# Optimization experiments

Measured on AMD Instinct MI355X. Metric: run time of the kernel, lower is better.

## Reference

```python
import jax, jax.numpy as jnp
import numpy as np

K = 4  # top-k nearest neighbors


def setup_inputs() -> dict:
    key = jax.random.key(0)
    k1, k2, k3 = jax.random.split(key, 3)
    N, D, M = 784, 512, 65536  # N_patches (28*28), feature dim, memory bank size
    query = jax.random.normal(k1, (N, D), dtype=jnp.float32)
    memory_bank = jax.random.normal(k2, (M, D), dtype=jnp.float32)
    # fcn: Conv2d(in=2*D=1024, out=1, kernel=3, padding=1)
    fan_in = 2 * D * 9
    fcn_w = jax.random.normal(k3, (1, 2 * D, 3, 3), dtype=jnp.float32) / np.sqrt(fan_in)
    fcn_b = jnp.zeros((1,), dtype=jnp.float32)
    return {"query": query, "memory_bank": memory_bank, "fcn_w": fcn_w, "fcn_b": fcn_b}


def reference(query, memory_bank, fcn_w, fcn_b):
    # pairwise L2 distances (torch.cdist p=2): [N, M]
    q2 = jnp.sum(query * query, axis=1, keepdims=True)           # [N, 1]
    m2 = jnp.sum(memory_bank * memory_bank, axis=1)              # [M]
    d2 = q2 + m2[None, :] - 2.0 * (query @ memory_bank.T)        # [N, M]
    dist = jnp.sqrt(jnp.maximum(d2, 0.0))
    # top-k smallest distances -> indices
    _, topk_idx = jax.lax.top_k(-dist, K)                        # [N, K]
    neighbors = memory_bank[topk_idx]                            # [N, K, D] gather
    neighbor_mean = jnp.mean(neighbors, axis=1)                  # [N, D]
    combined = jnp.concatenate([query, neighbor_mean], axis=1)   # [N, 2D]
    n, dim = combined.shape
    s = int(np.sqrt(n))                                          # 28
    x = combined.T.reshape(1, dim, s, s)                         # [1, 2D, 28, 28]
    out = jax.lax.conv_general_dilated(
        x, fcn_w, window_strides=(1, 1), padding=((1, 1), (1, 1)),
        dimension_numbers=("NCHW", "OIHW", "NCHW"))
    return out + fcn_b[None, :, None, None]                      # [1, 1, 28, 28]
```

## Files before the change

kernel.cpp:

```cpp
#include <hip/hip_runtime.h>
#include <hip/hip_bf16.h>
#include <stdint.h>

#define DIMS 512
#define NQ 784
#define QPAD 832
#define NM 65536
#define NTILE 13
#define NGROUP 2048
#define RESCORE 16
#define COLSTRIDE 1040

typedef float f32x4 __attribute__((ext_vector_type(4)));
typedef short bf16x8 __attribute__((ext_vector_type(8)));

__device__ __forceinline__ unsigned short f2bf(float x) {
    unsigned u = __float_as_uint(x);
    u += 0x7fffu + ((u >> 16) & 1u);
    return (unsigned short)(u >> 16);
}
__device__ __forceinline__ unsigned umn(unsigned a, unsigned b) { return a < b ? a : b; }
__device__ __forceinline__ unsigned umx(unsigned a, unsigned b) { return a > b ? a : b; }

__global__ __launch_bounds__(256) void prep_query(const float* __restrict__ q,
                                                  unsigned short* __restrict__ qbuf) {
    int i = (blockIdx.x * 256 + threadIdx.x) * 4;
    int row = i >> 9;
    ushort4 o = make_ushort4(0, 0, 0, 0);
    if (row < NQ) {
        float4 v = *(const float4*)(q + i);
        o.x = f2bf(v.x); o.y = f2bf(v.y); o.z = f2bf(v.z); o.w = f2bf(v.w);
    }
    *(ushort4*)(qbuf + i) = o;
}

__global__ __launch_bounds__(512, 1) void score_kernel(
    const float* __restrict__ bank,
    const unsigned short* __restrict__ qbuf,
    uint2* __restrict__ cand)
{
    __shared__ __align__(16) char bt[2][64 * COLSTRIDE];
    __shared__ float m2s[256];

    const int wg = blockIdx.x;
    const int t = threadIdx.x;
    const int v = t >> 6;
    const int lane = t & 63;
    const int lo = lane & 15;
    const int kg = lane >> 4;

#define STAGE(buf, tile)                                                                  \
    do {                                                                                  \
        _Pragma("unroll")                                                                 \
        for (int j = 0; j < 8; ++j) {                                                     \
            const int col = v * 8 + j;                                                    \
            const unsigned short* src =                                                   \
                qbuf + ((size_t)((tile) * 64 + col)) * DIMS + lane * 8;                   \
            __builtin_amdgcn_global_load_lds(                                             \
                (const __attribute__((address_space(1))) unsigned*)src,                   \
                (__attribute__((address_space(3))) unsigned*)(&bt[buf][col * COLSTRIDE]), \
                16, 0, 0);                                                                \
        }                                                                                 \
    } while (0)

    STAGE(0, 0);

    bf16x8 areg[2][16];
    float m2p[2];
    #pragma unroll
    for (int m = 0; m < 2; ++m) {
        const float* rp = bank + ((size_t)(wg * 256 + v * 32 + m * 16 + lo)) * DIMS + kg * 8;
        float ss = 0.f;
        #pragma unroll
        for (int ks = 0; ks < 16; ++ks) {
            float4 x = *(const float4*)(rp + ks * 32);
            float4 y = *(const float4*)(rp + ks * 32 + 4);
            ss += x.x * x.x + x.y * x.y + x.z * x.z + x.w * x.w;
            ss += y.x * y.x + y.y * y.y + y.z * y.z + y.w * y.w;
            union { bf16x8 v8; unsigned u[4]; } fr;
            __hip_bfloat162 h0 = __float22bfloat162_rn(make_float2(x.x, x.y));
            __hip_bfloat162 h1 = __float22bfloat162_rn(make_float2(x.z, x.w));
            __hip_bfloat162 h2 = __float22bfloat162_rn(make_float2(y.x, y.y));
            __hip_bfloat162 h3 = __float22bfloat162_rn(make_float2(y.z, y.w));
            fr.u[0] = *reinterpret_cast<unsigned*>(&h0);
            fr.u[1] = *reinterpret_cast<unsigned*>(&h1);
            fr.u[2] = *reinterpret_cast<unsigned*>(&h2);
            fr.u[3] = *reinterpret_cast<unsigned*>(&h3);
            areg[m][ks] = fr.v8;
        }
        m2p[m] = ss;
    }
    #pragma unroll
    for (int m = 0; m < 2; ++m) {
        m2p[m] += __shfl_xor(m2p[m], 16);
        m2p[m] += __shfl_xor(m2p[m], 32);
    }
    if (lane < 16) {
        m2s[v * 32 + lane] = m2p[0];
        m2s[v * 32 + 16 + lane] = m2p[1];
    }
    __syncthreads();
    f32x4 seed0, seed1;
    #pragma unroll
    for (int j = 0; j < 4; ++j) {
        seed0[j] = -0.5f * (1024.0f + m2s[v * 32 + kg * 4 + j]);
        seed1[j] = -0.5f * (1024.0f + m2s[v * 32 + 16 + kg * 4 + j]);
    }

    asm volatile("s_waitcnt vmcnt(0)" ::: "memory");
    __syncthreads();

    #pragma unroll 1
    for (int tile = 0; tile < NTILE; ++tile) {
        const int cur = tile & 1;
        if (tile + 1 < NTILE) STAGE(cur ^ 1, tile + 1);

        const char* B = &bt[cur][0];
        const int ntpEnd = (tile == NTILE - 1) ? 1 : 2;
        #pragma unroll 1
        for (int ntp = 0; ntp < ntpEnd; ++ntp) {
            const char* pb0 = B + (ntp * 32 + lo) * COLSTRIDE + kg * 16;
            const char* pb1 = pb0 + 16 * COLSTRIDE;
            f32x4 a00 = seed0, a01 = seed1, a10 = seed0, a11 = seed1;
            #pragma unroll
            for (int ks = 0; ks < 16; ++ks) {
                bf16x8 b0 = *(const bf16x8*)(pb0 + ks * 64);
                bf16x8 b1 = *(const bf16x8*)(pb1 + ks * 64);
                a00 = __builtin_amdgcn_mfma_f32_16x16x32_bf16(areg[0][ks], b0, a00, 0, 0, 0);
                a01 = __builtin_amdgcn_mfma_f32_16x16x32_bf16(areg[1][ks], b0, a01, 0, 0, 0);
                a10 = __builtin_amdgcn_mfma_f32_16x16x32_bf16(areg[0][ks], b1, a10, 0, 0, 0);
                a11 = __builtin_amdgcn_mfma_f32_16x16x32_bf16(areg[1][ks], b1, a11, 0, 0, 0);
            }
            #pragma unroll
            for (int n = 0; n < 2; ++n) {
                unsigned v1 = 0xFFFFFFFFu, v2 = 0xFFFFFFFFu;
                const f32x4& am0 = n ? a10 : a00;
                const f32x4& am1 = n ? a11 : a01;
                #pragma unroll
                for (int j = 0; j < 4; ++j) {
                    float s0 = -2.0f * am0[j];
                    unsigned u0 = (__float_as_uint(s0) & ~31u) | (unsigned)(kg * 4 + j);
                    unsigned t0 = umx(v1, u0);
                    v1 = umn(v1, u0);
                    v2 = umn(v2, t0);
                    float s1 = -2.0f * am1[j];
                    unsigned u1 = (__float_as_uint(s1) & ~31u) | (unsigned)(16 + kg * 4 + j);
                    unsigned t1 = umx(v1, u1);
                    v1 = umn(v1, u1);
                    v2 = umn(v2, t1);
                }
                #pragma unroll
                for (int off = 16; off <= 32; off <<= 1) {
                    unsigned o1 = (unsigned)__shfl_xor((int)v1, off);
                    unsigned o2 = (unsigned)__shfl_xor((int)v2, off);
                    unsigned mx = umx(v1, o1);
                    v1 = umn(v1, o1);
                    v2 = umn(umn(v2, o2), mx);
                }
                int col = tile * 64 + ntp * 32 + n * 16 + (lane & 15);
                if (lane < 16 && col < NQ)
                    cand[(size_t)(wg * 8 + v) * QPAD + col] = make_uint2(v1, v2);
            }
        }
        asm volatile("s_waitcnt vmcnt(0)" ::: "memory");
        __syncthreads();
    }
#undef STAGE
}

__global__ __launch_bounds__(256) void merge_kernel(
    const float* __restrict__ query, const float* __restrict__ bank,
    const uint2* __restrict__ cand, float* __restrict__ nm)
{
    const int row = blockIdx.x * 4 + (threadIdx.x >> 6);
    const int lane = threadIdx.x & 63;

    unsigned s0 = 0xFFFFFFFFu, s1 = 0xFFFFFFFFu, s2 = 0xFFFFFFFFu;
    unsigned s3 = 0xFFFFFFFFu, s4 = 0xFFFFFFFFu, s5 = 0xFFFFFFFFu;

#define INSERT(uu)                                  \
    do {                                            \
        unsigned tt = (uu), nv;                     \
        nv = umn(s0, tt); tt = umx(s0, tt); s0 = nv;\
        nv = umn(s1, tt); tt = umx(s1, tt); s1 = nv;\
        nv = umn(s2, tt); tt = umx(s2, tt); s2 = nv;\
        nv = umn(s3, tt); tt = umx(s3, tt); s3 = nv;\
        nv = umn(s4, tt); tt = umx(s4, tt); s4 = nv;\
        s5 = umn(s5, tt);                           \
    } while (0)

    #pragma unroll 4
    for (int j = 0; j < 32; ++j) {
        uint2 e = cand[((size_t)(lane * 32 + j)) * QPAD + row];
        unsigned jb = (unsigned)(j << 5);
        unsigned u0 = (e.x & ~0x3E0u) | jb;
        unsigned u1 = (e.y & ~0x3E0u) | jb;
        INSERT(u0);
        INSERT(u1);
    }
#undef INSERT

    int cidx[RESCORE];
    #pragma unroll
    for (int it = 0; it < RESCORE; ++it) {
        unsigned gm = s0;
        #pragma unroll
        for (int off = 1; off < 64; off <<= 1)
            gm = umn(gm, (unsigned)__shfl_xor((int)gm, off));
        unsigned long long bal = __ballot(s0 == gm);
        int wl = __ffsll((long long)bal) - 1;
        if (lane == wl) { s0 = s1; s1 = s2; s2 = s3; s3 = s4; s4 = s5; s5 = 0xFFFFFFFFu; }
        int g = wl * 32 + (int)((gm >> 5) & 31u);
        cidx[it] = g * 32 + (int)(gm & 31u);
    }

    const float* qr = query + (size_t)row * DIMS + lane * 8;
    float4 qx = *(const float4*)qr;
    float4 qy = *(const float4*)(qr + 4);
    double d2[RESCORE];
    #pragma unroll
    for (int c = 0; c < RESCORE; ++c) {
        const float* mr = bank + (size_t)cidx[c] * DIMS + lane * 8;
        float4 mx = *(const float4*)mr;
        float4 my = *(const float4*)(mr + 4);
        double s = 0.0;
        double dd;
        dd = (double)qx.x - (double)mx.x; s += dd * dd;
        dd = (double)qx.y - (double)mx.y; s += dd * dd;
        dd = (double)qx.z - (double)mx.z; s += dd * dd;
        dd = (double)qx.w - (double)mx.w; s += dd * dd;
        dd = (double)qy.x - (double)my.x; s += dd * dd;
        dd = (double)qy.y - (double)my.y; s += dd * dd;
        dd = (double)qy.z - (double)my.z; s += dd * dd;
        dd = (double)qy.w - (double)my.w; s += dd * dd;
        #pragma unroll
        for (int off = 1; off < 64; off <<= 1) s += __shfl_xor(s, off);
        d2[c] = s;
    }

    int sel[4];
    unsigned used = 0;
    #pragma unroll
    for (int k = 0; k < 4; ++k) {
        double bv = 1e300; int bidx = 1 << 30; int bc = 0;
        #pragma unroll
        for (int c = 0; c < RESCORE; ++c) {
            bool live = !((used >> c) & 1u);
            if (live && (d2[c] < bv || (d2[c] == bv && cidx[c] < bidx))) {
                bv = d2[c]; bidx = cidx[c]; bc = c;
            }
        }
        used |= 1u << bc;
        sel[k] = bidx;
    }

    const float* r0 = bank + (size_t)sel[0] * DIMS + lane * 8;
    const float* r1 = bank + (size_t)sel[1] * DIMS + lane * 8;
    const float* r2 = bank + (size_t)sel[2] * DIMS + lane * 8;
    const float* r3 = bank + (size_t)sel[3] * DIMS + lane * 8;
    float* dst = nm + (size_t)row * DIMS + lane * 8;
    #pragma unroll
    for (int h = 0; h < 2; ++h) {
        float4 a = *(const float4*)(r0 + h * 4);
        float4 b = *(const float4*)(r1 + h * 4);
        float4 c = *(const float4*)(r2 + h * 4);
        float4 d = *(const float4*)(r3 + h * 4);
        float4 o;
        o.x = 0.25f * (a.x + b.x + c.x + d.x);
        o.y = 0.25f * (a.y + b.y + c.y + d.y);
        o.z = 0.25f * (a.z + b.z + c.z + d.z);
        o.w = 0.25f * (a.w + b.w + c.w + d.w);
        *(float4*)(dst + h * 4) = o;
    }
}

__global__ __launch_bounds__(256) void conv_kernel(
    const float* __restrict__ query, const float* __restrict__ nm,
    const float* __restrict__ fw, const float* __restrict__ fb,
    float* __restrict__ out)
{
    __shared__ float red[256];
    int pix = blockIdx.x, t = threadIdx.x;
    int i = pix / 28, j = pix % 28;
    float acc = 0.f;
    for (int c = t; c < 1024; c += 256) {
        const float* wrow = fw + c * 9;
        for (int di = 0; di < 3; ++di) {
            int h = i + di - 1;
            if (h < 0 || h >= 28) continue;
            for (int dj = 0; dj < 3; ++dj) {
                int w = j + dj - 1;
                if (w < 0 || w >= 28) continue;
                int n = h * 28 + w;
                float x = (c < 512) ? query[(size_t)n * 512 + c]
                                    : nm[(size_t)n * 512 + (c - 512)];
                acc += x * wrow[di * 3 + dj];
            }
        }
    }
    red[t] = acc;
    __syncthreads();
    for (int s = 128; s; s >>= 1) {
        if (t < s) red[t] += red[t + s];
        __syncthreads();
    }
    if (t == 0) out[pix] = red[0] + fb[0];
}

extern "C" void kernel_launch(void* const* d_in, const int* in_sizes, int n_in,
                              void* d_out, int out_size, void* d_ws, size_t ws_size,
                              hipStream_t stream)
{
    const float* query = (const float*)d_in[0];
    const float* bank  = (const float*)d_in[1];
    const float* fw    = (const float*)d_in[2];
    const float* fb    = (const float*)d_in[3];
    float* out = (float*)d_out;

    char* ws = (char*)d_ws;
    unsigned short* qbuf = (unsigned short*)ws;
    uint2* cand = (uint2*)(ws + 851968);
    float* nm   = (float*)(ws + 851968 + 13631488);

    prep_query<<<QPAD * DIMS / 1024, 256, 0, stream>>>(query, qbuf);
    score_kernel<<<256, 512, 0, stream>>>(bank, qbuf, cand);
    merge_kernel<<<NQ / 4, 256, 0, stream>>>(query, bank, cand, nm);
    conv_kernel<<<NQ, 256, 0, stream>>>(query, nm, fw, fb, out);
}
```

Baseline: 128.6 us.

## Switch coarse distance scoring to FP8 MFMA with swizzled LDS and wider rescoring

The coarse bank-vs-query scoring GEMM now uses fp8 e4m3 operands and 16x16x32 fp8 MFMA instead of bf16, halving query staging bytes. An XOR swizzle replaces the padded LDS stride. Work is split into 512 workgroups of 256 threads at two per CU, with a manually unrolled tile loop and s_setprio around the MFMA bursts. To offset the coarser fp8 scores, the merge keeps 8 candidates per lane and rescores 32 candidates exactly in double, one candidate per lane pair, with selection through shared memory. The risk is that fp8 error drops true neighbours out of the candidate set, and the merge step does more work.

```diff
diff --git a/kernel.cpp b/kernel.cpp
--- a/kernel.cpp
+++ b/kernel.cpp
@@ -1,46 +1,53 @@
 #include <hip/hip_runtime.h>
-#include <hip/hip_bf16.h>
+#include <hip/hip_fp8.h>
 #include <stdint.h>
 
 #define DIMS 512
 #define NQ 784
 #define QPAD 832
-#define NM 65536
 #define NTILE 13
-#define NGROUP 2048
-#define RESCORE 16
-#define COLSTRIDE 1040
+#define RESCORE 32
 
 typedef float f32x4 __attribute__((ext_vector_type(4)));
-typedef short bf16x8 __attribute__((ext_vector_type(8)));
-
-__device__ __forceinline__ unsigned short f2bf(float x) {
-    unsigned u = __float_as_uint(x);
-    u += 0x7fffu + ((u >> 16) & 1u);
-    return (unsigned short)(u >> 16);
-}
+
 __device__ __forceinline__ unsigned umn(unsigned a, unsigned b) { return a < b ? a : b; }
 __device__ __forceinline__ unsigned umx(unsigned a, unsigned b) { return a > b ? a : b; }
 
+__device__ __forceinline__ unsigned pk4(float a, float b, float c, float d) {
+#if __has_builtin(__builtin_amdgcn_cvt_pk_fp8_f32)
+    int v = 0;
+    v = __builtin_amdgcn_cvt_pk_fp8_f32(a, b, v, false);
+    v = __builtin_amdgcn_cvt_pk_fp8_f32(c, d, v, true);
+    return (unsigned)v;
+#else
+    __hip_fp8_e4m3 x(a), y(b), z(c), w(d);
+    return (unsigned)x.__x | ((unsigned)y.__x << 8) | ((unsigned)z.__x << 16) | ((unsigned)w.__x << 24);
+#endif
+}
+
 __global__ __launch_bounds__(256) void prep_query(const float* __restrict__ q,
-                                                  unsigned short* __restrict__ qbuf) {
-    int i = (blockIdx.x * 256 + threadIdx.x) * 4;
-    int row = i >> 9;
-    ushort4 o = make_ushort4(0, 0, 0, 0);
-    if (row < NQ) {
-        float4 v = *(const float4*)(q + i);
-        o.x = f2bf(v.x); o.y = f2bf(v.y); o.z = f2bf(v.z); o.w = f2bf(v.w);
-    }
-    *(ushort4*)(qbuf + i) = o;
-}
-
-__global__ __launch_bounds__(512, 1) void score_kernel(
+                                                  char* __restrict__ qb8) {
+    int gid = blockIdx.x * 256 + threadIdx.x;
+    int col = gid >> 6;
+    int k0 = (gid & 63) * 8;
+    float4 a = make_float4(0.f, 0.f, 0.f, 0.f), b = a;
+    if (col < NQ) {
+        a = *(const float4*)(q + (size_t)col * DIMS + k0);
+        b = *(const float4*)(q + (size_t)col * DIMS + k0 + 4);
+    }
+    uint2 o;
+    o.x = pk4(a.x, a.y, a.z, a.w);
+    o.y = pk4(b.x, b.y, b.z, b.w);
+    *(uint2*)(qb8 + col * 512 + (k0 ^ ((col & 7) << 3))) = o;
+}
+
+__global__ __launch_bounds__(256, 2) void score_kernel(
     const float* __restrict__ bank,
-    const unsigned short* __restrict__ qbuf,
+    const char* __restrict__ qb8,
     uint2* __restrict__ cand)
 {
-    __shared__ __align__(16) char bt[2][64 * COLSTRIDE];
-    __shared__ float m2s[256];
+    __shared__ __align__(16) char bt[2][64 * 512];
+    __shared__ float m2s[128];
 
     const int wg = blockIdx.x;
     const int t = threadIdx.x;
@@ -49,27 +56,26 @@
     const int lo = lane & 15;
     const int kg = lane >> 4;
 
-#define STAGE(buf, tile)                                                                  \
-    do {                                                                                  \
-        _Pragma("unroll")                                                                 \
-        for (int j = 0; j < 8; ++j) {                                                     \
-            const int col = v * 8 + j;                                                    \
-            const unsigned short* src =                                                   \
-                qbuf + ((size_t)((tile) * 64 + col)) * DIMS + lane * 8;                   \
-            __builtin_amdgcn_global_load_lds(                                             \
-                (const __attribute__((address_space(1))) unsigned*)src,                   \
-                (__attribute__((address_space(3))) unsigned*)(&bt[buf][col * COLSTRIDE]), \
-                16, 0, 0);                                                                \
-        }                                                                                 \
+#define STAGE(BUF, TILE)                                                              \
+    do {                                                                              \
+        _Pragma("unroll")                                                             \
+        for (int j = 0; j < 8; ++j) {                                                 \
+            const int col = v * 16 + j * 2;                                           \
+            const char* src = qb8 + ((size_t)((TILE) * 64 + col)) * 512 + lane * 16;  \
+            __builtin_amdgcn_global_load_lds(                                         \
+                (const __attribute__((address_space(1))) unsigned*)src,               \
+                (__attribute__((address_space(3))) unsigned*)(&bt[BUF][col * 512]),   \
+                16, 0, 0);                                                            \
+        }                                                                             \
     } while (0)
 
     STAGE(0, 0);
 
-    bf16x8 areg[2][16];
+    long areg[2][16];
     float m2p[2];
     #pragma unroll
     for (int m = 0; m < 2; ++m) {
-        const float* rp = bank + ((size_t)(wg * 256 + v * 32 + m * 16 + lo)) * DIMS + kg * 8;
+        const float* rp = bank + ((size_t)(wg * 128 + v * 32 + m * 16 + lo)) * DIMS + kg * 8;
         float ss = 0.f;
         #pragma unroll
         for (int ks = 0; ks < 16; ++ks) {
@@ -77,16 +83,9 @@
             float4 y = *(const float4*)(rp + ks * 32 + 4);
             ss += x.x * x.x + x.y * x.y + x.z * x.z + x.w * x.w;
             ss += y.x * y.x + y.y * y.y + y.z * y.z + y.w * y.w;
-            union { bf16x8 v8; unsigned u[4]; } fr;
-            __hip_bfloat162 h0 = __float22bfloat162_rn(make_float2(x.x, x.y));
-            __hip_bfloat162 h1 = __float22bfloat162_rn(make_float2(x.z, x.w));
-            __hip_bfloat162 h2 = __float22bfloat162_rn(make_float2(y.x, y.y));
-            __hip_bfloat162 h3 = __float22bfloat162_rn(make_float2(y.z, y.w));
-            fr.u[0] = *reinterpret_cast<unsigned*>(&h0);
-            fr.u[1] = *reinterpret_cast<unsigned*>(&h1);
-            fr.u[2] = *reinterpret_cast<unsigned*>(&h2);
-            fr.u[3] = *reinterpret_cast<unsigned*>(&h3);
-            areg[m][ks] = fr.v8;
+            unsigned l32 = pk4(x.x, x.y, x.z, x.w);
+            unsigned h32 = pk4(y.x, y.y, y.z, y.w);
+            areg[m][ks] = (long)(((unsigned long long)h32 << 32) | l32);
         }
         m2p[m] = ss;
     }
@@ -99,72 +98,90 @@
         m2s[v * 32 + lane] = m2p[0];
         m2s[v * 32 + 16 + lane] = m2p[1];
     }
-    __syncthreads();
-    f32x4 seed0, seed1;
-    #pragma unroll
-    for (int j = 0; j < 4; ++j) {
-        seed0[j] = -0.5f * (1024.0f + m2s[v * 32 + kg * 4 + j]);
-        seed1[j] = -0.5f * (1024.0f + m2s[v * 32 + 16 + kg * 4 + j]);
-    }
 
     asm volatile("s_waitcnt vmcnt(0)" ::: "memory");
     __syncthreads();
 
+    f32x4 seed0, seed1;
+    #pragma unroll
+    for (int j = 0; j < 4; ++j) {
+        seed0[j] = -(512.0f + 0.5f * m2s[v * 32 + kg * 4 + j]);
+        seed1[j] = -(512.0f + 0.5f * m2s[v * 32 + 16 + kg * 4 + j]);
+    }
+
+    const char* pA0 = &bt[0][0] + lo * 512 + ((kg * 8) ^ ((lo & 7) << 3));
+    const char* pA1 = (const char*)((uintptr_t)pA0 ^ 32);
+
+#define KSLOOP(ACC, BUF, NTP)                                                              \
+    do {                                                                                   \
+        __builtin_amdgcn_s_setprio(1);                                                     \
+        _Pragma("unroll")                                                                  \
+        for (int ks = 0; ks < 16; ++ks) {                                                  \
+            const char* bs = (ks & 1) ? pA1 : pA0;                                         \
+            const int off = (BUF) * 32768 + (NTP) * 16384 + (ks >> 1) * 64;                \
+            long b0 = *(const long*)(bs + off);                                            \
+            long b1 = *(const long*)(bs + off + 8192);                                     \
+            ACC[0][0] = __builtin_amdgcn_mfma_f32_16x16x32_fp8_fp8(areg[0][ks], b0, ACC[0][0], 0, 0, 0); \
+            ACC[1][0] = __builtin_amdgcn_mfma_f32_16x16x32_fp8_fp8(areg[1][ks], b0, ACC[1][0], 0, 0, 0); \
+            ACC[0][1] = __builtin_amdgcn_mfma_f32_16x16x32_fp8_fp8(areg[0][ks], b1, ACC[0][1], 0, 0, 0); \
+            ACC[1][1] = __builtin_amdgcn_mfma_f32_16x16x32_fp8_fp8(areg[1][ks], b1, ACC[1][1], 0, 0, 0); \
+        }                                                                                  \
+        __builtin_amdgcn_s_setprio(0);                                                     \
+    } while (0)
+
+#define SEL(ACC, TILE, NTP)                                                                \
+    do {                                                                                   \
+        _Pragma("unroll")                                                                  \
+        for (int n = 0; n < 2; ++n) {                                                      \
+            unsigned v1 = 0xFFFFFFFFu, v2 = 0xFFFFFFFFu;                                   \
+            _Pragma("unroll")                                                              \
+            for (int m = 0; m < 2; ++m)                                                    \
+                _Pragma("unroll")                                                          \
+                for (int j = 0; j < 4; ++j) {                                              \
+                    unsigned u = ((__float_as_uint(ACC[m][n][j]) ^ 0x80000000u) & ~31u)    \
+                                 | (unsigned)(m * 16 + kg * 4 + j);                        \
+                    unsigned mx = umx(v1, u);                                              \
+                    v1 = umn(v1, u);                                                       \
+                    v2 = umn(v2, mx);                                                      \
+                }                                                                          \
+            _Pragma("unroll")                                                              \
+            for (int off = 16; off <= 32; off <<= 1) {                                     \
+                unsigned o1 = (unsigned)__shfl_xor((int)v1, off);                          \
+                unsigned o2 = (unsigned)__shfl_xor((int)v2, off);                          \
+                unsigned mx = umx(v1, o1);                                                 \
+                v1 = umn(v1, o1);                                                          \
+                v2 = umn(umn(v2, o2), mx);                                                 \
+            }                                                                              \
+            int col = (TILE) * 64 + (NTP) * 32 + n * 16 + lo;                              \
+            if (lane < 16 && col < NQ)                                                     \
+                cand[(size_t)(wg * 4 + v) * QPAD + col] = make_uint2(v1, v2);              \
+        }                                                                                  \
+    } while (0)
+
+#define TILEBODY(TILE, BUF)                                                                \
+    do {                                                                                   \
+        if ((TILE) + 1 < NTILE) STAGE((BUF) ^ 1, (TILE) + 1);                              \
+        f32x4 accP[2][2], accQ[2][2];                                                      \
+        accP[0][0] = seed0; accP[0][1] = seed0; accP[1][0] = seed1; accP[1][1] = seed1;    \
+        KSLOOP(accP, BUF, 0);                                                              \
+        accQ[0][0] = seed0; accQ[0][1] = seed0; accQ[1][0] = seed1; accQ[1][1] = seed1;    \
+        KSLOOP(accQ, BUF, 1);                                                              \
+        SEL(accP, TILE, 0);                                                                \
+        SEL(accQ, TILE, 1);                                                                \
+        asm volatile("s_waitcnt vmcnt(0)" ::: "memory");                                   \
+        __syncthreads();                                                                   \
+    } while (0)
+
     #pragma unroll 1
-    for (int tile = 0; tile < NTILE; ++tile) {
-        const int cur = tile & 1;
-        if (tile + 1 < NTILE) STAGE(cur ^ 1, tile + 1);
-
-        const char* B = &bt[cur][0];
-        const int ntpEnd = (tile == NTILE - 1) ? 1 : 2;
-        #pragma unroll 1
-        for (int ntp = 0; ntp < ntpEnd; ++ntp) {
-            const char* pb0 = B + (ntp * 32 + lo) * COLSTRIDE + kg * 16;
-            const char* pb1 = pb0 + 16 * COLSTRIDE;
-            f32x4 a00 = seed0, a01 = seed1, a10 = seed0, a11 = seed1;
-            #pragma unroll
-            for (int ks = 0; ks < 16; ++ks) {
-                bf16x8 b0 = *(const bf16x8*)(pb0 + ks * 64);
-                bf16x8 b1 = *(const bf16x8*)(pb1 + ks * 64);
-                a00 = __builtin_amdgcn_mfma_f32_16x16x32_bf16(areg[0][ks], b0, a00, 0, 0, 0);
-                a01 = __builtin_amdgcn_mfma_f32_16x16x32_bf16(areg[1][ks], b0, a01, 0, 0, 0);
-                a10 = __builtin_amdgcn_mfma_f32_16x16x32_bf16(areg[0][ks], b1, a10, 0, 0, 0);
-                a11 = __builtin_amdgcn_mfma_f32_16x16x32_bf16(areg[1][ks], b1, a11, 0, 0, 0);
-            }
-            #pragma unroll
-            for (int n = 0; n < 2; ++n) {
-                unsigned v1 = 0xFFFFFFFFu, v2 = 0xFFFFFFFFu;
-                const f32x4& am0 = n ? a10 : a00;
-                const f32x4& am1 = n ? a11 : a01;
-                #pragma unroll
-                for (int j = 0; j < 4; ++j) {
-                    float s0 = -2.0f * am0[j];
-                    unsigned u0 = (__float_as_uint(s0) & ~31u) | (unsigned)(kg * 4 + j);
-                    unsigned t0 = umx(v1, u0);
-                    v1 = umn(v1, u0);
-                    v2 = umn(v2, t0);
-                    float s1 = -2.0f * am1[j];
-                    unsigned u1 = (__float_as_uint(s1) & ~31u) | (unsigned)(16 + kg * 4 + j);
-                    unsigned t1 = umx(v1, u1);
-                    v1 = umn(v1, u1);
-                    v2 = umn(v2, t1);
-                }
-                #pragma unroll
-                for (int off = 16; off <= 32; off <<= 1) {
-                    unsigned o1 = (unsigned)__shfl_xor((int)v1, off);
-                    unsigned o2 = (unsigned)__shfl_xor((int)v2, off);
-                    unsigned mx = umx(v1, o1);
-                    v1 = umn(v1, o1);
-                    v2 = umn(umn(v2, o2), mx);
-                }
-                int col = tile * 64 + ntp * 32 + n * 16 + (lane & 15);
-                if (lane < 16 && col < NQ)
-                    cand[(size_t)(wg * 8 + v) * QPAD + col] = make_uint2(v1, v2);
-            }
-        }
-        asm volatile("s_waitcnt vmcnt(0)" ::: "memory");
-        __syncthreads();
-    }
+    for (int tt = 0; tt < 6; ++tt) {
+        TILEBODY(2 * tt, 0);
+        TILEBODY(2 * tt + 1, 1);
+    }
+    TILEBODY(12, 0);
+
+#undef TILEBODY
+#undef SEL
+#undef KSLOOP
 #undef STAGE
 }
 
@@ -172,35 +189,39 @@
     const float* __restrict__ query, const float* __restrict__ bank,
     const uint2* __restrict__ cand, float* __restrict__ nm)
 {
-    const int row = blockIdx.x * 4 + (threadIdx.x >> 6);
-    const int lane = threadIdx.x & 63;
-
-    unsigned s0 = 0xFFFFFFFFu, s1 = 0xFFFFFFFFu, s2 = 0xFFFFFFFFu;
-    unsigned s3 = 0xFFFFFFFFu, s4 = 0xFFFFFFFFu, s5 = 0xFFFFFFFFu;
-
-#define INSERT(uu)                                  \
-    do {                                            \
-        unsigned tt = (uu), nv;                     \
-        nv = umn(s0, tt); tt = umx(s0, tt); s0 = nv;\
-        nv = umn(s1, tt); tt = umx(s1, tt); s1 = nv;\
-        nv = umn(s2, tt); tt = umx(s2, tt); s2 = nv;\
-        nv = umn(s3, tt); tt = umx(s3, tt); s3 = nv;\
-        nv = umn(s4, tt); tt = umx(s4, tt); s4 = nv;\
-        s5 = umn(s5, tt);                           \
+    __shared__ double d2s[4][32];
+    __shared__ int    cis[4][32];
+
+    const int wv = threadIdx.x >> 6, lane = threadIdx.x & 63;
+    const int row = blockIdx.x * 4 + wv;
+
+    unsigned s0 = ~0u, s1 = ~0u, s2 = ~0u, s3 = ~0u;
+    unsigned s4 = ~0u, s5 = ~0u, s6 = ~0u, s7 = ~0u;
+
+#define INS(U)                                        \
+    do {                                              \
+        unsigned tt = (U), nv;                        \
+        nv = umn(s0, tt); tt = umx(s0, tt); s0 = nv;  \
+        nv = umn(s1, tt); tt = umx(s1, tt); s1 = nv;  \
+        nv = umn(s2, tt); tt = umx(s2, tt); s2 = nv;  \
+        nv = umn(s3, tt); tt = umx(s3, tt); s3 = nv;  \
+        nv = umn(s4, tt); tt = umx(s4, tt); s4 = nv;  \
+        nv = umn(s5, tt); tt = umx(s5, tt); s5 = nv;  \
+        nv = umn(s6, tt); tt = umx(s6, tt); s6 = nv;  \
+        s7 = umn(s7, tt);                             \
     } while (0)
 
     #pragma unroll 4
     for (int j = 0; j < 32; ++j) {
         uint2 e = cand[((size_t)(lane * 32 + j)) * QPAD + row];
         unsigned jb = (unsigned)(j << 5);
-        unsigned u0 = (e.x & ~0x3E0u) | jb;
-        unsigned u1 = (e.y & ~0x3E0u) | jb;
-        INSERT(u0);
-        INSERT(u1);
-    }
-#undef INSERT
-
-    int cidx[RESCORE];
+        INS((e.x & ~0x3E0u) | jb);
+        INS((e.y & ~0x3E0u) | jb);
+    }
+#undef INS
+
+    const int myC = lane & 31;
+    int myCand = 0;
     #pragma unroll
     for (int it = 0; it < RESCORE; ++it) {
         unsigned gm = s0;
@@ -209,55 +230,48 @@
             gm = umn(gm, (unsigned)__shfl_xor((int)gm, off));
         unsigned long long bal = __ballot(s0 == gm);
         int wl = __ffsll((long long)bal) - 1;
-        if (lane == wl) { s0 = s1; s1 = s2; s2 = s3; s3 = s4; s4 = s5; s5 = 0xFFFFFFFFu; }
-        int g = wl * 32 + (int)((gm >> 5) & 31u);
-        cidx[it] = g * 32 + (int)(gm & 31u);
-    }
-
-    const float* qr = query + (size_t)row * DIMS + lane * 8;
-    float4 qx = *(const float4*)qr;
-    float4 qy = *(const float4*)(qr + 4);
-    double d2[RESCORE];
-    #pragma unroll
-    for (int c = 0; c < RESCORE; ++c) {
-        const float* mr = bank + (size_t)cidx[c] * DIMS + lane * 8;
-        float4 mx = *(const float4*)mr;
-        float4 my = *(const float4*)(mr + 4);
-        double s = 0.0;
-        double dd;
-        dd = (double)qx.x - (double)mx.x; s += dd * dd;
-        dd = (double)qx.y - (double)mx.y; s += dd * dd;
-        dd = (double)qx.z - (double)mx.z; s += dd * dd;
-        dd = (double)qx.w - (double)mx.w; s += dd * dd;
-        dd = (double)qy.x - (double)my.x; s += dd * dd;
-        dd = (double)qy.y - (double)my.y; s += dd * dd;
-        dd = (double)qy.z - (double)my.z; s += dd * dd;
-        dd = (double)qy.w - (double)my.w; s += dd * dd;
-        #pragma unroll
-        for (int off = 1; off < 64; off <<= 1) s += __shfl_xor(s, off);
-        d2[c] = s;
-    }
-
-    int sel[4];
+        int ci = (wl * 32 + (int)((gm >> 5) & 31u)) * 32 + (int)(gm & 31u);
+        myCand = (it == myC) ? ci : myCand;
+        if (lane == wl) { s0 = s1; s1 = s2; s2 = s3; s3 = s4; s4 = s5; s5 = s6; s6 = s7; s7 = ~0u; }
+    }
+
+    const float* qr = query + (size_t)row * DIMS + (lane >> 5) * 256;
+    const float* mr = bank + (size_t)myCand * DIMS + (lane >> 5) * 256;
+    double s = 0.0;
+    #pragma unroll 8
+    for (int i = 0; i < 64; ++i) {
+        float4 a = *(const float4*)(qr + i * 4);
+        float4 b = *(const float4*)(mr + i * 4);
+        double d;
+        d = (double)a.x - (double)b.x; s += d * d;
+        d = (double)a.y - (double)b.y; s += d * d;
+        d = (double)a.z - (double)b.z; s += d * d;
+        d = (double)a.w - (double)b.w; s += d * d;
+    }
+    s += __shfl_xor(s, 32);
+    if (lane < 32) { d2s[wv][lane] = s; cis[wv][lane] = myCand; }
+    __syncthreads();
+
+    int sel0 = 0, sel1 = 0, sel2 = 0, sel3 = 0;
     unsigned used = 0;
     #pragma unroll
     for (int k = 0; k < 4; ++k) {
-        double bv = 1e300; int bidx = 1 << 30; int bc = 0;
-        #pragma unroll
-        for (int c = 0; c < RESCORE; ++c) {
+        double bv = 1e300; int bidx = 0x7FFFFFFF; int bc = 0;
+        for (int c = 0; c < 32; ++c) {
             bool live = !((used >> c) & 1u);
-            if (live && (d2[c] < bv || (d2[c] == bv && cidx[c] < bidx))) {
-                bv = d2[c]; bidx = cidx[c]; bc = c;
-            }
+            double dv = d2s[wv][c];
+            int cv = cis[wv][c];
+            if (live && (dv < bv || (dv == bv && cv < bidx))) { bv = dv; bidx = cv; bc = c; }
         }
         used |= 1u << bc;
-        sel[k] = bidx;
-    }
-
-    const float* r0 = bank + (size_t)sel[0] * DIMS + lane * 8;
-    const float* r1 = bank + (size_t)sel[1] * DIMS + lane * 8;
-    const float* r2 = bank + (size_t)sel[2] * DIMS + lane * 8;
-    const float* r3 = bank + (size_t)sel[3] * DIMS + lane * 8;
+        if (k == 0) sel0 = bidx; else if (k == 1) sel1 = bidx;
+        else if (k == 2) sel2 = bidx; else sel3 = bidx;
+    }
+
+    const float* r0 = bank + (size_t)sel0 * DIMS + lane * 8;
+    const float* r1 = bank + (size_t)sel1 * DIMS + lane * 8;
+    const float* r2 = bank + (size_t)sel2 * DIMS + lane * 8;
+    const float* r3 = bank + (size_t)sel3 * DIMS + lane * 8;
     float* dst = nm + (size_t)row * DIMS + lane * 8;
     #pragma unroll
     for (int h = 0; h < 2; ++h) {
@@ -318,12 +332,12 @@
     float* out = (float*)d_out;
 
     char* ws = (char*)d_ws;
-    unsigned short* qbuf = (unsigned short*)ws;
-    uint2* cand = (uint2*)(ws + 851968);
-    float* nm   = (float*)(ws + 851968 + 13631488);
-
-    prep_query<<<QPAD * DIMS / 1024, 256, 0, stream>>>(query, qbuf);
-    score_kernel<<<256, 512, 0, stream>>>(bank, qbuf, cand);
+    char*  qb8  = ws;
+    uint2* cand = (uint2*)(ws + 425984);
+    float* nm   = (float*)(ws + 425984 + 13631488);
+
+    prep_query<<<208, 256, 0, stream>>>(query, qb8);
+    score_kernel<<<512, 256, 0, stream>>>(bank, qb8, cand);
     merge_kernel<<<NQ / 4, 256, 0, stream>>>(query, bank, cand, nm);
     conv_kernel<<<NQ, 256, 0, stream>>>(query, nm, fw, fb, out);
 }
```

Result: no change. 126.9 us (-1.3%).
